# Kernel tuning notes

Hardware: AMD Instinct MI355X
Metric: run time of the kernel (lower is better)

## Reference

```python
import jax, jax.numpy as jnp
import numpy as np
from functools import partial

BLUR_K = 5
SIGMA = 1.5
DOWN = 4
SCALE = 5.0
OFFSET = 0.2

_DN = ('NCHW', 'OIHW', 'NCHW')


def _gaussian_kernel(k, sigma):
    x = jnp.arange(k, dtype=jnp.float32) - (k - 1) / 2.0
    g = jnp.exp(-x ** 2 / (2.0 * sigma ** 2))
    g2 = jnp.outer(g, g)
    g2 = g2 / g2.sum()
    return g2.reshape(1, 1, k, k)


def setup_inputs() -> dict:
    key = jax.random.key(0)
    left_rgb = jax.random.uniform(key, (16, 3, 544, 960), dtype=jnp.float32)
    return {"left_rgb": left_rgb}


def reference(left_rgb):
    B, C, H, W = left_rgb.shape
    # rgb -> gray (1x1 conv with fixed weights)
    w = jnp.array([0.2989, 0.587, 0.114], dtype=left_rgb.dtype)
    gray = jnp.einsum('bchw,c->bhw', left_rgb, w)[:, None]  # [B,1,H,W]

    # gaussian blur with reflect padding (torch F.pad mode='reflect')
    pad = BLUR_K // 2
    gray_p = jnp.pad(gray, ((0, 0), (0, 0), (pad, pad), (pad, pad)), mode='reflect')
    gk = _gaussian_kernel(BLUR_K, SIGMA).astype(left_rgb.dtype)
    gray_smooth = jax.lax.conv_general_dilated(gray_p, gk, (1, 1), 'VALID',
                                               dimension_numbers=_DN)

    # sobel gradients (cross-correlation, zero padding=1, same as torch conv2d)
    sx = jnp.array([[-1., 0., 1.], [-2., 0., 2.], [-1., 0., 1.]],
                   dtype=left_rgb.dtype).reshape(1, 1, 3, 3)
    sy = jnp.array([[-1., -2., -1.], [0., 0., 0.], [1., 2., 1.]],
                   dtype=left_rgb.dtype).reshape(1, 1, 3, 3)
    gx = jax.lax.conv_general_dilated(gray_smooth, sx, (1, 1), [(1, 1), (1, 1)],
                                      dimension_numbers=_DN)
    gy = jax.lax.conv_general_dilated(gray_smooth, sy, (1, 1), [(1, 1), (1, 1)],
                                      dimension_numbers=_DN)
    mag = jnp.sqrt(gx ** 2 + gy ** 2 + 1e-6)  # [B,1,H,W]

    # avg_pool2d kernel=stride=DOWN (H, W divisible by DOWN)
    down = mag.reshape(B, 1, H // DOWN, DOWN, W // DOWN, DOWN).mean(axis=(3, 5))

    edge_mask = jax.nn.sigmoid(SCALE * (down - OFFSET)) ** 2.0
    return edge_mask
```

## Files before the change

### kernel.cpp

```cpp
#include <hip/hip_runtime.h>
#include <cmath>

constexpr int B = 16, C = 3, H = 544, W = 960;
constexpr int OH = 136, OW = 240;
constexpr size_t HW = (size_t)H * W;

constexpr int TOH = 8, TOW = 30, NTH = 17, NTW = 8, MH = 32, MW = 120;
constexpr int GR = 40;
constexpr int GS = 132;
constexpr int NT = 5;

__global__ __launch_bounds__(256, 2)
void edge_fused(const float* __restrict__ in, float* __restrict__ out,
                float gn0, float gn1, float gn2)
{
    __shared__ float gray[GR * GS];

    const int tid = threadIdx.x;
    const int blk = blockIdx.x;
    const int tw = blk % NTW;
    const int th = (blk / NTW) % NTH;
    const int b  = blk / (NTW * NTH);
    const int mh0 = th * MH, mw0 = tw * MW;
    const float* inb = in + (size_t)b * C * HW;

    float4 Rv[NT], Gv[NT], Bv[NT];
    #pragma unroll
    for (int k = 0; k < NT; ++k) {
        const int idx = tid + 256 * k;
        const int r = idx >> 5;
        const int c = idx & 31;
        int g = mh0 - 4 + r;
        g = g < 0 ? -g : (g >= H ? 2 * H - 2 - g : g);
        int gcb = mw0 - 4 + 4 * c;
        gcb = gcb < 0 ? 0 : (gcb > W - 4 ? W - 4 : gcb);
        const float* p = inb + (size_t)g * W + gcb;
        Rv[k] = *reinterpret_cast<const float4*>(p);
        Gv[k] = *reinterpret_cast<const float4*>(p + HW);
        Bv[k] = *reinterpret_cast<const float4*>(p + 2 * HW);
    }
    #pragma unroll
    for (int k = 0; k < NT; ++k) {
        const int idx = tid + 256 * k;
        const int r = idx >> 5;
        const int c = idx & 31;
        float4 g;
        g.x = fmaf(0.2989f, Rv[k].x, fmaf(0.587f, Gv[k].x, 0.114f * Bv[k].x));
        g.y = fmaf(0.2989f, Rv[k].y, fmaf(0.587f, Gv[k].y, 0.114f * Bv[k].y));
        g.z = fmaf(0.2989f, Rv[k].z, fmaf(0.587f, Gv[k].z, 0.114f * Bv[k].z));
        g.w = fmaf(0.2989f, Rv[k].w, fmaf(0.587f, Gv[k].w, 0.114f * Bv[k].w));
        const bool edgeq = (tw == 0 && c == 0) || (tw == NTW - 1 && c == 31);
        if (!edgeq)
            *reinterpret_cast<float4*>(&gray[r * GS + 4 * c]) = g;
    }
    if ((tw == 0 || tw == NTW - 1) && tid < GR) {
        const int r = tid;
        const int c = (tw == 0) ? 0 : 31;
        int g = mh0 - 4 + r;
        g = g < 0 ? -g : (g >= H ? 2 * H - 2 - g : g);
        float4 gv;
        float* gp = &gv.x;
        #pragma unroll
        for (int m = 0; m < 4; ++m) {
            int gc = mw0 - 4 + 4 * c + m;
            gc = gc < 0 ? -gc : (gc >= W ? 2 * W - 2 - gc : gc);
            const float* p = inb + (size_t)g * W + gc;
            gp[m] = 0.2989f * p[0] + 0.587f * p[HW] + 0.114f * p[2 * HW];
        }
        *reinterpret_cast<float4*>(&gray[r * GS + 4 * c]) = gv;
    }
    __syncthreads();

    if (tid < TOH * TOW) {
        const int orow = tid / TOW;
        const int ocol = tid - orow * TOW;
        const int lc0 = 4 * ocol;
        const int rb = 4 * orow + 1;

        float sm6[6][6];
        #pragma unroll
        for (int i = 0; i < 6; ++i)
            #pragma unroll
            for (int j = 0; j < 6; ++j) sm6[i][j] = 0.f;

        const float gk[5] = {gn0, gn1, gn2, gn1, gn0};
        #pragma unroll
        for (int tr = 0; tr < 10; ++tr) {
            const float* p = &gray[(rb + tr) * GS + lc0];
            const float4 u = *reinterpret_cast<const float4*>(p);
            const float4 v = *reinterpret_cast<const float4*>(p + 4);
            const float4 w = *reinterpret_cast<const float4*>(p + 8);
            const float t12[12] = {u.x, u.y, u.z, u.w, v.x, v.y, v.z, v.w,
                                   w.x, w.y, w.z, w.w};
            float h6[6];
            #pragma unroll
            for (int j = 0; j < 6; ++j)
                h6[j] = fmaf(gn0, t12[1 + j] + t12[5 + j],
                        fmaf(gn1, t12[2 + j] + t12[4 + j], gn2 * t12[3 + j]));
            #pragma unroll
            for (int i = 0; i < 6; ++i) {
                const int m = tr - i;
                if (m >= 0 && m < 5) {
                    #pragma unroll
                    for (int j = 0; j < 6; ++j)
                        sm6[i][j] = fmaf(gk[m], h6[j], sm6[i][j]);
                }
            }
        }

        #pragma unroll
        for (int i = 0; i < 6; ++i) {
            const int hh = mh0 + 4 * orow - 1 + i;
            const float rm = (hh >= 0 && hh < H) ? 1.f : 0.f;
            #pragma unroll
            for (int j = 0; j < 6; ++j) {
                const int ww = mw0 + 4 * ocol - 1 + j;
                sm6[i][j] *= rm * ((ww >= 0 && ww < W) ? 1.f : 0.f);
            }
        }

        float acc[4] = {0.f, 0.f, 0.f, 0.f};
        #pragma unroll
        for (int i = 0; i < 4; ++i) {
            #pragma unroll
            for (int j = 0; j < 4; ++j) {
                const float a00 = sm6[i][j],     a01 = sm6[i][j + 1],     a02 = sm6[i][j + 2];
                const float a10 = sm6[i + 1][j],                          a12 = sm6[i + 1][j + 2];
                const float a20 = sm6[i + 2][j], a21 = sm6[i + 2][j + 1], a22 = sm6[i + 2][j + 2];
                const float gx = (a02 - a00) + 2.f * (a12 - a10) + (a22 - a20);
                const float gy = (a20 + 2.f * a21 + a22) - (a00 + 2.f * a01 + a02);
                acc[i] += sqrtf(gx * gx + gy * gy + 1e-6f);
            }
        }
        const float down = ((acc[0] + acc[1]) + (acc[2] + acc[3])) * (1.f / 16.f);
        const float x = 5.0f * (down - 0.2f);
        const float sg = 1.f / (1.f + __expf(-x));
        const size_t o = ((size_t)b * OH + (th * TOH + orow)) * OW + (tw * TOW + ocol);
        out[o] = sg * sg;
    }
}

extern "C" void kernel_launch(void* const* d_in, const int* in_sizes, int n_in,
                              void* d_out, int out_size, void* d_ws, size_t ws_size,
                              hipStream_t stream) {
    const float* in = (const float*)d_in[0];
    float* out = (float*)d_out;

    const double g0 = std::exp(-4.0 / 4.5);
    const double g1 = std::exp(-1.0 / 4.5);
    const double g2 = 1.0;
    const double S = 2.0 * (g0 + g1) + g2;
    const float gn0 = (float)(g0 / S);
    const float gn1 = (float)(g1 / S);
    const float gn2 = (float)(g2 / S);

    hipLaunchKernelGGL(edge_fused, dim3(B * NTH * NTW), dim3(256), 0, stream,
                       in, out, gn0, gn1, gn2);
}
```

Before: 33.54 us.

## Swizzle block order across XCDs, build reflect borders via shuffles, raise compute priority

```diff
diff --git a/kernel.cpp b/kernel.cpp
--- a/kernel.cpp
+++ b/kernel.cpp
@@ -9,6 +9,8 @@
 constexpr int GR = 40;
 constexpr int GS = 132;
 constexpr int NT = 5;
+constexpr int NBLK = B * NTH * NTW;
+constexpr int CPX = NBLK / 8;
 
 __global__ __launch_bounds__(256, 2)
 void edge_fused(const float* __restrict__ in, float* __restrict__ out,
@@ -17,7 +19,7 @@
     __shared__ float gray[GR * GS];
 
     const int tid = threadIdx.x;
-    const int blk = blockIdx.x;
+    const int blk = (blockIdx.x & 7) * CPX + (blockIdx.x >> 3);
     const int tw = blk % NTW;
     const int th = (blk / NTW) % NTH;
     const int b  = blk / (NTW * NTH);
@@ -52,25 +54,22 @@
         const bool edgeq = (tw == 0 && c == 0) || (tw == NTW - 1 && c == 31);
         if (!edgeq)
             *reinterpret_cast<float4*>(&gray[r * GS + 4 * c]) = g;
-    }
-    if ((tw == 0 || tw == NTW - 1) && tid < GR) {
-        const int r = tid;
-        const int c = (tw == 0) ? 0 : 31;
-        int g = mh0 - 4 + r;
-        g = g < 0 ? -g : (g >= H ? 2 * H - 2 - g : g);
-        float4 gv;
-        float* gp = &gv.x;
-        #pragma unroll
-        for (int m = 0; m < 4; ++m) {
-            int gc = mw0 - 4 + 4 * c + m;
-            gc = gc < 0 ? -gc : (gc >= W ? 2 * W - 2 - gc : gc);
-            const float* p = inb + (size_t)g * W + gc;
-            gp[m] = 0.2989f * p[0] + 0.587f * p[HW] + 0.114f * p[2 * HW];
+
+        if (tw == 0) {
+            const float nx = __shfl_down(g.x, 1, 32);
+            if (c == 1)
+                *reinterpret_cast<float4*>(&gray[r * GS]) =
+                    make_float4(nx, g.w, g.z, g.y);
+        } else if (tw == NTW - 1) {
+            const float pw = __shfl_up(g.w, 1, 32);
+            if (c == 30)
+                *reinterpret_cast<float4*>(&gray[r * GS + 4 * 31]) =
+                    make_float4(g.z, g.y, g.x, pw);
         }
-        *reinterpret_cast<float4*>(&gray[r * GS + 4 * c]) = gv;
     }
     __syncthreads();
 
+    __builtin_amdgcn_s_setprio(1);
     if (tid < TOH * TOW) {
         const int orow = tid / TOW;
         const int ocol = tid - orow * TOW;
@@ -138,6 +137,7 @@
         const size_t o = ((size_t)b * OH + (th * TOH + orow)) * OW + (tw * TOW + ocol);
         out[o] = sg * sg;
     }
+    __builtin_amdgcn_s_setprio(0);
 }
 
 extern "C" void kernel_launch(void* const* d_in, const int* in_sizes, int n_in,
@@ -154,6 +154,6 @@
     const float gn1 = (float)(g1 / S);
     const float gn2 = (float)(g2 / S);
 
-    hipLaunchKernelGGL(edge_fused, dim3(B * NTH * NTW), dim3(256), 0, stream,
+    hipLaunchKernelGGL(edge_fused, dim3(NBLK), dim3(256), 0, stream,
                        in, out, gn0, gn1, gn2);
 }
```

Result: faster. 31.75 us (-5.3%).
